# Kernel optimization log

Measured on AMD Instinct MI355X. Metric: run time of the kernel, lower is better.

Reference implementation:

```python
import jax, jax.numpy as jnp
import numpy as np
import math

B, H, S, D = 2, 16, 2048, 64
NEG = -1000000000.0

def setup_inputs() -> dict:
    key = jax.random.key(0)
    kq, kk, kv, km = jax.random.split(key, 4)
    query = jax.random.normal(kq, (B, H, S, D), dtype=jnp.float32)
    k_ = jax.random.normal(kk, (B, H, S, D), dtype=jnp.float32)
    value = jax.random.normal(kv, (B, H, S, D), dtype=jnp.float32)
    mask = jax.random.randint(km, (B, 1, S, S), 0, 2, dtype=jnp.int32)
    return {"query": query, "key": k_, "value": value, "mask": mask}

def reference(query, key, value, mask):
    # scores: [B,H,S,S]
    scale = 1.0 / math.sqrt(query.shape[-1])
    scores = jnp.einsum('bhqd,bhkd->bhqk', query, key) * scale
    scores = jnp.where(mask == 0, NEG, scores)
    # NOTE: original code uses F.softmax(scores, dim=1) -> softmax over the
    # HEAD axis (axis=1) for 4D inputs. Reproduced faithfully.
    p_attn = jax.nn.softmax(scores, axis=1)
    out = jnp.einsum('bhqk,bhkd->bhqd', p_attn, value)
    return (out, p_attn)
```

## Files before the change

kernel.cpp:

```cpp
#include <hip/hip_runtime.h>
#include <hip/hip_bf16.h>
#include <stdint.h>

#define B_ 2
#define H_ 16
#define S_ 2048
#define D_ 64

typedef __attribute__((ext_vector_type(8))) short bf16x8;
typedef __attribute__((ext_vector_type(4))) float f32x4;
typedef __attribute__((ext_vector_type(4))) unsigned short u16x4;

__device__ __forceinline__ short f2bf(float x){
  union { float f; uint32_t u; } v; v.f = x;
  uint32_t r = v.u + 0x7FFFu + ((v.u >> 16) & 1u);
  return (short)(r >> 16);
}
__device__ __forceinline__ float bf2f(short s){
  union { uint32_t u; float f; } v; v.u = ((uint32_t)(uint16_t)s) << 16;
  return v.f;
}

__global__ __launch_bounds__(256) void cast_k(const float* __restrict__ K,
                                              short* __restrict__ Khi,
                                              short* __restrict__ Klo){
  size_t idx = ((size_t)blockIdx.x * 256 + threadIdx.x) * 8;
  float4 a = *(const float4*)(K + idx);
  float4 b = *(const float4*)(K + idx + 4);
  float v[8] = {a.x,a.y,a.z,a.w,b.x,b.y,b.z,b.w};
  bf16x8 vh, vl;
  #pragma unroll
  for (int i = 0; i < 8; ++i){
    short hi = f2bf(v[i]);
    vh[i] = hi;
    vl[i] = f2bf(v[i] - bf2f(hi));
  }
  *(bf16x8*)(Khi + idx) = vh;
  *(bf16x8*)(Klo + idx) = vl;
}

__global__ __launch_bounds__(256) void transpose_v(const float* __restrict__ V,
                                                   short* __restrict__ Vt){
  __shared__ float T[64][65];
  int bh = blockIdx.x >> 5;
  int k0 = (blockIdx.x & 31) * 64;
  int t = threadIdx.x;
  {
    int col = (t & 15) * 4;
    #pragma unroll
    for (int i = 0; i < 4; ++i){
      int row = (t >> 4) + i * 16;
      float4 a = *(const float4*)(V + ((size_t)bh * S_ + k0 + row) * D_ + col);
      T[col+0][row] = a.x; T[col+1][row] = a.y; T[col+2][row] = a.z; T[col+3][row] = a.w;
    }
  }
  __syncthreads();
  {
    int d  = t >> 2;
    int kk = (t & 3) * 16;
    bf16x8 o0, o1;
    #pragma unroll
    for (int j = 0; j < 8; ++j){
      o0[j] = f2bf(T[d][kk + j]);
      o1[j] = f2bf(T[d][kk + 8 + j]);
    }
    short* dst = Vt + ((size_t)bh * D_ + d) * S_ + k0 + kk;
    *(bf16x8*)(dst)     = o0;
    *(bf16x8*)(dst + 8) = o1;
  }
}

__global__ __launch_bounds__(1024, 4) void attn_main(
    const float* __restrict__ Q, const short* __restrict__ Khi,
    const short* __restrict__ Klo, const short* __restrict__ Vt,
    const int* __restrict__ mask, float* __restrict__ out,
    float* __restrict__ pout)
{
  __shared__ unsigned short sc[2][H_][1024];
  __shared__ float zb[2][1024];
  __shared__ float cb[2][1024];

  const int tid  = threadIdx.x;
  const int h    = tid >> 6;
  const int lane = tid & 63;
  const int g    = lane >> 4;
  const int lr   = lane & 15;

  const int b  = blockIdx.x >> 7;
  const int q0 = (blockIdx.x & 127) << 4;
  const int nIt = S_ / 64;

  const size_t bh = (size_t)b * H_ + h;

  bf16x8 qhi[2], qlo[2];
  {
    const float* qp = Q + (bh * S_ + q0 + lr) * D_ + g * 8;
    #pragma unroll
    for (int c = 0; c < 2; ++c){
      float4 a  = *(const float4*)(qp + c*32);
      float4 d4 = *(const float4*)(qp + c*32 + 4);
      float v[8] = {a.x,a.y,a.z,a.w,d4.x,d4.y,d4.z,d4.w};
      #pragma unroll
      for (int i = 0; i < 8; ++i){
        short hi = f2bf(v[i]);
        qhi[c][i] = hi;
        qlo[c][i] = f2bf(v[i] - bf2f(hi));
      }
    }
  }

  f32x4 o[4];
  #pragma unroll
  for (int j = 0; j < 4; ++j) o[j] = (f32x4){0.f,0.f,0.f,0.f};

  const int swzq = 4 * (lr & 7);

  const short* kbase_hi = Khi + (bh * S_ + lr) * D_ + g * 8;
  const short* kbase_lo = Klo + (bh * S_ + lr) * D_ + g * 8;
  const short* vbase    = Vt  + (bh * D_ + lr) * S_ + g * 8;
  float*       pbase    = pout + (bh * S_ + q0 + lr) * S_ + g * 8;

  const int* mp = mask + ((size_t)b * S_ + q0 + (tid >> 6)) * S_ + (tid & 63);
  int mreg = mp[0];

  for (int it = 0; it < nIt; ++it){
    const int k0  = it * 64;
    const int buf = it & 1;

    int mnext = 0;
    if (it + 1 < nIt) mnext = mp[(it + 1) * 64];

    f32x4 s[4];
    #pragma unroll
    for (int t = 0; t < 4; ++t){
      s[t] = (f32x4){0.f,0.f,0.f,0.f};
      #pragma unroll
      for (int c = 0; c < 2; ++c){
        bf16x8 kh = *(const bf16x8*)(kbase_hi + (size_t)(k0 + 16*t) * D_ + c*32);
        bf16x8 kl = *(const bf16x8*)(kbase_lo + (size_t)(k0 + 16*t) * D_ + c*32);
        s[t] = __builtin_amdgcn_mfma_f32_16x16x32_bf16(qhi[c], kh, s[t], 0, 0, 0);
        s[t] = __builtin_amdgcn_mfma_f32_16x16x32_bf16(qlo[c], kh, s[t], 0, 0, 0);
        s[t] = __builtin_amdgcn_mfma_f32_16x16x32_bf16(qhi[c], kl, s[t], 0, 0, 0);
      }
    }
    #pragma unroll
    for (int t = 0; t < 4; ++t){
      #pragma unroll
      for (int r = 0; r < 4; ++r){
        int q = 4*g + r;
        int k = 16*t + lr;
        float e = __expf(s[t][r] * 0.125f);
        sc[buf][h][q*64 + (k ^ (4*(q&7)))] = (unsigned short)f2bf(e);
      }
    }
    __syncthreads();

    {
      int q = tid >> 6, k = tid & 63;
      int ks = q*64 + (k ^ (4*(q&7)));
      float dsum = 0.f;
      #pragma unroll
      for (int hh = 0; hh < H_; ++hh) dsum += bf2f((short)sc[buf][hh][ks]);
      zb[buf][ks] = mreg ? (1.0f / dsum) : 0.0f;
      cb[buf][ks] = mreg ? 0.0f : 0.0625f;
    }
    __syncthreads();

    {
      const unsigned short* sp = &sc[buf][h][lr*64];
      const float* zp = &zb[buf][lr*64];
      const float* cp = &cb[buf][lr*64];
      bf16x8 pa[2];
      #pragma unroll
      for (int m = 0; m < 2; ++m){
        int b1 = (32*m + 8*g) ^ swzq;
        int b2 = b1 ^ 4;
        u16x4 eh0 = *(const u16x4*)(sp + b1);
        u16x4 eh1 = *(const u16x4*)(sp + b2);
        f32x4 z0 = *(const f32x4*)(zp + b1);
        f32x4 z1 = *(const f32x4*)(zp + b2);
        f32x4 c0 = *(const f32x4*)(cp + b1);
        f32x4 c1 = *(const f32x4*)(cp + b2);
        float p[8];
        #pragma unroll
        for (int j = 0; j < 4; ++j){
          p[j]     = bf2f((short)eh0[j]) * z0[j] + c0[j];
          p[4 + j] = bf2f((short)eh1[j]) * z1[j] + c1[j];
        }
        f32x4 p0 = {p[0],p[1],p[2],p[3]};
        f32x4 p1 = {p[4],p[5],p[6],p[7]};
        *(f32x4*)(pbase + k0 + 32*m)     = p0;
        *(f32x4*)(pbase + k0 + 32*m + 4) = p1;
        #pragma unroll
        for (int i = 0; i < 8; ++i) pa[m][i] = f2bf(p[i]);
      }

      #pragma unroll
      for (int j = 0; j < 4; ++j){
        bf16x8 vb0 = *(const bf16x8*)(vbase + (size_t)(16*j) * S_ + k0);
        bf16x8 vb1 = *(const bf16x8*)(vbase + (size_t)(16*j) * S_ + k0 + 32);
        o[j] = __builtin_amdgcn_mfma_f32_16x16x32_bf16(pa[0], vb0, o[j], 0, 0, 0);
        o[j] = __builtin_amdgcn_mfma_f32_16x16x32_bf16(pa[1], vb1, o[j], 0, 0, 0);
      }
    }
    mreg = mnext;
  }

  #pragma unroll
  for (int j = 0; j < 4; ++j){
    #pragma unroll
    for (int r = 0; r < 4; ++r){
      out[(bh * S_ + q0 + 4*g + r) * D_ + 16*j + lr] = o[j][r];
    }
  }
}

extern "C" void kernel_launch(void* const* d_in, const int* in_sizes, int n_in,
                              void* d_out, int out_size, void* d_ws, size_t ws_size,
                              hipStream_t stream){
  const float* Q    = (const float*)d_in[0];
  const float* K    = (const float*)d_in[1];
  const float* V    = (const float*)d_in[2];
  const int*   mask = (const int*)d_in[3];

  const size_t nkv = (size_t)B_ * H_ * S_ * D_;

  short* Khi = (short*)d_ws;
  short* Klo = Khi + nkv;
  short* Vt  = Klo + nkv;

  float* out  = (float*)d_out;
  float* pout = out + nkv;

  cast_k<<<(int)(nkv / (256 * 8)), 256, 0, stream>>>(K, Khi, Klo);
  transpose_v<<<B_ * H_ * (S_ / 64), 256, 0, stream>>>(V, Vt);
  attn_main<<<B_ * (S_ / 16), 1024, 0, stream>>>(Q, Khi, Klo, Vt, mask, out, pout);
}
```

Measured before the change: 541.1 us.

## Coalesce p_attn stores with nontemporal writes, prefetch V, use LDS-only barriers

Rewrites the p_attn output store so each wave writes contiguous 256-byte row segments, with lanes spanning keys instead of rows, and uses nontemporal stores. The 16.8M-element probability tensor is the dominant memory traffic, and these stores are meant to cut write transactions and cache pollution. V loads for the iteration are hoisted to the loop start so they overlap the QK MFMAs. Barriers become a custom macro that waits only on lgkmcnt, so outstanding global loads need not drain. The unswizzled zb/cb layout adds a second LDS read pass and raises register pressure.

```diff
diff --git a/kernel.cpp b/kernel.cpp
--- a/kernel.cpp
+++ b/kernel.cpp
@@ -20,6 +20,13 @@
   union { uint32_t u; float f; } v; v.u = ((uint32_t)(uint16_t)s) << 16;
   return v.f;
 }
+
+#define LDS_BARRIER() do {                                  \
+  __builtin_amdgcn_sched_barrier(0);                        \
+  asm volatile("s_waitcnt lgkmcnt(0)" ::: "memory");        \
+  __builtin_amdgcn_s_barrier();                             \
+  __builtin_amdgcn_sched_barrier(0);                        \
+} while (0)
 
 __global__ __launch_bounds__(256) void cast_k(const float* __restrict__ K,
                                               short* __restrict__ Khi,
@@ -118,7 +125,7 @@
   const short* kbase_hi = Khi + (bh * S_ + lr) * D_ + g * 8;
   const short* kbase_lo = Klo + (bh * S_ + lr) * D_ + g * 8;
   const short* vbase    = Vt  + (bh * D_ + lr) * S_ + g * 8;
-  float*       pbase    = pout + (bh * S_ + q0 + lr) * S_ + g * 8;
+  float*       pstbase  = pout + (bh * S_ + q0 + g) * S_ + 4 * lr;
 
   const int* mp = mask + ((size_t)b * S_ + q0 + (tid >> 6)) * S_ + (tid & 63);
   int mreg = mp[0];
@@ -126,6 +133,14 @@
   for (int it = 0; it < nIt; ++it){
     const int k0  = it * 64;
     const int buf = it & 1;
+
+    bf16x8 vreg[4][2];
+    #pragma unroll
+    for (int j = 0; j < 4; ++j){
+      #pragma unroll
+      for (int m = 0; m < 2; ++m)
+        vreg[j][m] = *(const bf16x8*)(vbase + (size_t)(16*j) * S_ + k0 + 32*m);
+    }
 
     int mnext = 0;
     if (it + 1 < nIt) mnext = mp[(it + 1) * 64];
@@ -153,7 +168,7 @@
         sc[buf][h][q*64 + (k ^ (4*(q&7)))] = (unsigned short)f2bf(e);
       }
     }
-    __syncthreads();
+    LDS_BARRIER();
 
     {
       int q = tid >> 6, k = tid & 63;
@@ -161,11 +176,26 @@
       float dsum = 0.f;
       #pragma unroll
       for (int hh = 0; hh < H_; ++hh) dsum += bf2f((short)sc[buf][hh][ks]);
-      zb[buf][ks] = mreg ? (1.0f / dsum) : 0.0f;
-      cb[buf][ks] = mreg ? 0.0f : 0.0625f;
-    }
-    __syncthreads();
-
+      zb[buf][q*64 + k] = mreg ? (1.0f / dsum) : 0.0f;
+      cb[buf][q*64 + k] = mreg ? 0.0f : 0.0625f;
+    }
+    LDS_BARRIER();
+
+    {
+      #pragma unroll
+      for (int st = 0; st < 4; ++st){
+        int q  = 4*st + g;
+        int ke = 4*lr;
+        int ksw = (ke) ^ (4*(q&7));
+        u16x4 ev = *(const u16x4*)&sc[buf][h][q*64 + ksw];
+        f32x4 zv = *(const f32x4*)&zb[buf][q*64 + ke];
+        f32x4 cv = *(const f32x4*)&cb[buf][q*64 + ke];
+        f32x4 pv;
+        #pragma unroll
+        for (int t2 = 0; t2 < 4; ++t2) pv[t2] = bf2f((short)ev[t2]) * zv[t2] + cv[t2];
+        __builtin_nontemporal_store(pv, (f32x4*)(pstbase + (size_t)(4*st) * S_ + k0));
+      }
+    }
     {
       const unsigned short* sp = &sc[buf][h][lr*64];
       const float* zp = &zb[buf][lr*64];
@@ -173,34 +203,28 @@
       bf16x8 pa[2];
       #pragma unroll
       for (int m = 0; m < 2; ++m){
-        int b1 = (32*m + 8*g) ^ swzq;
+        int kb = 32*m + 8*g;
+        int b1 = kb ^ swzq;
         int b2 = b1 ^ 4;
         u16x4 eh0 = *(const u16x4*)(sp + b1);
         u16x4 eh1 = *(const u16x4*)(sp + b2);
-        f32x4 z0 = *(const f32x4*)(zp + b1);
-        f32x4 z1 = *(const f32x4*)(zp + b2);
-        f32x4 c0 = *(const f32x4*)(cp + b1);
-        f32x4 c1 = *(const f32x4*)(cp + b2);
+        f32x4 z0 = *(const f32x4*)(zp + kb);
+        f32x4 z1 = *(const f32x4*)(zp + kb + 4);
+        f32x4 c0 = *(const f32x4*)(cp + kb);
+        f32x4 c1 = *(const f32x4*)(cp + kb + 4);
         float p[8];
         #pragma unroll
         for (int j = 0; j < 4; ++j){
           p[j]     = bf2f((short)eh0[j]) * z0[j] + c0[j];
           p[4 + j] = bf2f((short)eh1[j]) * z1[j] + c1[j];
         }
-        f32x4 p0 = {p[0],p[1],p[2],p[3]};
-        f32x4 p1 = {p[4],p[5],p[6],p[7]};
-        *(f32x4*)(pbase + k0 + 32*m)     = p0;
-        *(f32x4*)(pbase + k0 + 32*m + 4) = p1;
         #pragma unroll
         for (int i = 0; i < 8; ++i) pa[m][i] = f2bf(p[i]);
       }
-
       #pragma unroll
       for (int j = 0; j < 4; ++j){
-        bf16x8 vb0 = *(const bf16x8*)(vbase + (size_t)(16*j) * S_ + k0);
-        bf16x8 vb1 = *(const bf16x8*)(vbase + (size_t)(16*j) * S_ + k0 + 32);
-        o[j] = __builtin_amdgcn_mfma_f32_16x16x32_bf16(pa[0], vb0, o[j], 0, 0, 0);
-        o[j] = __builtin_amdgcn_mfma_f32_16x16x32_bf16(pa[1], vb1, o[j], 0, 0, 0);
+        o[j] = __builtin_amdgcn_mfma_f32_16x16x32_bf16(pa[0], vreg[j][0], o[j], 0, 0, 0);
+        o[j] = __builtin_amdgcn_mfma_f32_16x16x32_bf16(pa[1], vreg[j][1], o[j], 0, 0, 0);
       }
     }
     mreg = mnext;
```

New measurement: 634.9 us. 1.17x slower.
